# Optimization experiments

Measured on AMD Instinct MI355X. Metric: run time of the kernel, lower is better.

Reference implementation:

```python
import jax, jax.numpy as jnp
import numpy as np

HEAD_SIZE = 128
B, L = 4, 4096

def setup_inputs() -> dict:
    key = jax.random.key(0)
    k1, k2, k3 = jax.random.split(key, 3)
    return {
        "key": jax.random.normal(k1, (B, L, HEAD_SIZE), dtype=jnp.float32),
        "query": jax.random.normal(k2, (B, L, HEAD_SIZE), dtype=jnp.float32),
        "value": jax.random.normal(k3, (B, L, HEAD_SIZE), dtype=jnp.float32),
    }

def reference(key, query, value):
    # attention scores: [B, L, L]
    scale = 1.0 / jnp.sqrt(jnp.asarray(HEAD_SIZE, dtype=query.dtype))
    att = jnp.einsum("bqd,bkd->bqk", query, key) * scale
    # causal mask (tril): positions k > q get -inf
    causal = jnp.tril(jnp.ones((att.shape[1], att.shape[2]), dtype=bool))
    att = jnp.where(causal[None, :, :], att, jnp.array(-jnp.inf, dtype=att.dtype))
    logits = jax.nn.softmax(att, axis=-1)
    # dropout omitted (eval mode / deterministic reference)
    out = jnp.einsum("bqk,bkd->bqd", logits, value)
    return out
```

## Files before the change

kernel.cpp:

```cpp
#include <hip/hip_runtime.h>

#define BB 4
#define LL 4096
#define DD 128

typedef __attribute__((ext_vector_type(8))) short short8;
typedef __attribute__((ext_vector_type(4))) float f32x4;

typedef __attribute__((address_space(1))) const unsigned int gas_u32;
typedef __attribute__((address_space(3))) unsigned int las_u32;

__device__ __forceinline__ void gload_lds16(const void* g, void* l) {
  __builtin_amdgcn_global_load_lds((gas_u32*)g, (las_u32*)l, 16, 0, 0);
}

__device__ __forceinline__ unsigned short f2bf(float x) {
  union { float f; unsigned int u; } c; c.f = x;
  unsigned int r = (c.u + 0x7FFFu + ((c.u >> 16) & 1u)) >> 16;
  return (unsigned short)r;
}
__device__ __forceinline__ float bf2f(unsigned short h) {
  union { unsigned int u; float f; } c; c.u = (unsigned int)h << 16;
  return c.f;
}

__host__ __device__ __forceinline__ int slotBase(int p) {
  int g2 = (p - 4) >> 2, w2 = (p - 4) & 3;
  return 2 * g2 * g2 + 6 * g2 + w2 * (g2 + 2);
}

__global__ __launch_bounds__(256) void prep(const float* __restrict__ K,
                                            const float* __restrict__ V,
                                            unsigned short* __restrict__ Kb,
                                            unsigned short* __restrict__ Vt) {
  __shared__ unsigned short tile[64 * 130];
  int b  = blockIdx.x >> 6;
  int kt = (blockIdx.x & 63) << 6;
  int t = threadIdx.x;
  {
    int key = t >> 2, part = t & 3;
    const float* src = K + ((size_t)b * LL + kt + key) * DD + part * 32;
    unsigned short* dst = Kb + ((size_t)b * LL + kt + key) * DD + part * 32;
#pragma unroll
    for (int j = 0; j < 4; ++j) {
      float4 x = *(const float4*)(src + j * 8);
      float4 y = *(const float4*)(src + j * 8 + 4);
      union { unsigned short h[8]; uint4 v; } o;
      o.h[0] = f2bf(x.x); o.h[1] = f2bf(x.y); o.h[2] = f2bf(x.z); o.h[3] = f2bf(x.w);
      o.h[4] = f2bf(y.x); o.h[5] = f2bf(y.y); o.h[6] = f2bf(y.z); o.h[7] = f2bf(y.w);
      *(uint4*)(dst + j * 8) = o.v;
    }
  }
  int keyi = t >> 5, dim = (t & 31) * 4;
#pragma unroll
  for (int j = 0; j < 8; ++j) {
    int key = keyi + j * 8;
    float4 x = *(const float4*)(V + ((size_t)b * LL + kt + key) * DD + dim);
    uint2 pk;
    pk.x = f2bf(x.x) | ((unsigned int)f2bf(x.y) << 16);
    pk.y = f2bf(x.z) | ((unsigned int)f2bf(x.w) << 16);
    *(uint2*)(tile + key * 130 + dim) = pk;
  }
  __syncthreads();
  int kg = (t & 7) * 8, d0 = t >> 3;
#pragma unroll
  for (int j = 0; j < 4; ++j) {
    int d = d0 + j * 32;
    union { unsigned short h[8]; uint4 v; } o;
#pragma unroll
    for (int i = 0; i < 8; ++i) o.h[i] = tile[(kg + i) * 130 + d];
    *(uint4*)(Vt + ((size_t)b * DD + d) * LL + kt + kg) = o.v;
  }
}

__global__ __launch_bounds__(256, 3) void attn_fwd(const float* __restrict__ Q,
                                                   const unsigned short* __restrict__ Kb,
                                                   const unsigned short* __restrict__ Vt,
                                                   float* __restrict__ Out,
                                                   unsigned short* __restrict__ partO,
                                                   float* __restrict__ stats,
                                                   int split) {
  __shared__ unsigned short Ks[64 * 128];
  __shared__ unsigned short Vs[128 * 64];
  __shared__ unsigned short Ps[4][32 * 72];

  int tid = threadIdx.x;
  int wave = tid >> 6;
  int lane = tid & 63;
  int l = lane & 15, gq = lane >> 4;
  int lx = l & 7;

  int rem = (int)blockIdx.x, p = 31, nch;
  while (true) {
    nch = split ? ((2 * p + 2 + 7) >> 3) : 1;
    int n = 4 * nch;
    if (rem < n) break;
    rem -= n; --p;
  }
  int b = rem / nch, c = rem % nch;
  int T = 2 * p + 2;
  int nIters = split ? min(8, T - c * 8) : T;
  int ktBase = c << 9;
  int q0w = (p << 7) + wave * 32;
  int wkend = q0w + 31;
  int slot = (split && nch > 1) ? (b * 140 + slotBase(p) + c) : 0;

  const float SC = 0.08838834764831845f * 1.4426950408889634f;
  short8 qf[2][4];
#pragma unroll
  for (int mt = 0; mt < 2; ++mt) {
    const float* qp = Q + ((size_t)b * LL + q0w + mt * 16 + l) * DD + gq * 8;
#pragma unroll
    for (int cc = 0; cc < 4; ++cc) {
      float4 x = *(const float4*)(qp + cc * 32);
      float4 y = *(const float4*)(qp + cc * 32 + 4);
      short8 f;
      f[0] = (short)f2bf(x.x * SC); f[1] = (short)f2bf(x.y * SC);
      f[2] = (short)f2bf(x.z * SC); f[3] = (short)f2bf(x.w * SC);
      f[4] = (short)f2bf(y.x * SC); f[5] = (short)f2bf(y.y * SC);
      f[6] = (short)f2bf(y.z * SC); f[7] = (short)f2bf(y.w * SC);
      qf[mt][cc] = f;
    }
  }

  f32x4 acc[2][8];
#pragma unroll
  for (int mt = 0; mt < 2; ++mt)
#pragma unroll
    for (int i = 0; i < 8; ++i) acc[mt][i] = (f32x4){0.f, 0.f, 0.f, 0.f};
  f32x4 den[2];
  den[0] = (f32x4){0.f, 0.f, 0.f, 0.f};
  den[1] = (f32x4){0.f, 0.f, 0.f, 0.f};

  short8 ones;
#pragma unroll
  for (int j = 0; j < 8; ++j) ones[j] = (short)0x3F80;

  unsigned short* Pw = Ps[wave];
  const unsigned short* kgbase = Kb + (size_t)b * LL * DD;
  const unsigned short* vgbase = Vt + (size_t)b * DD * LL;

  for (int it = 0; it < nIters; ++it) {
    int kt = ktBase + it * 64;

    __syncthreads();
#pragma unroll
    for (int j = 0; j < 4; ++j) {
      int pk_ = j * 256 + tid;
      int krow = pk_ >> 4;
      int kcol = (pk_ & 15) ^ (krow & 7);
      gload_lds16(kgbase + (size_t)(kt + krow) * DD + kcol * 8, &Ks[pk_ * 8]);
      int vrow = pk_ >> 3;
      int vcol = (pk_ & 7) ^ (vrow & 7);
      gload_lds16(vgbase + (size_t)vrow * LL + kt + vcol * 8, &Vs[pk_ * 8]);
    }
    __syncthreads();

    if (kt > wkend) continue;

    bool diag = (kt + 63 > q0w);

#pragma unroll
    for (int nt = 0; nt < 4; ++nt) {
      const unsigned short* kp = Ks + (nt * 16 + l) * 128;
      f32x4 a0 = (f32x4){0.f, 0.f, 0.f, 0.f};
      f32x4 a1 = (f32x4){0.f, 0.f, 0.f, 0.f};
#pragma unroll
      for (int cc = 0; cc < 4; ++cc) {
        short8 kf = *(const short8*)(kp + (((gq + 4 * cc) ^ lx) << 3));
        a0 = __builtin_amdgcn_mfma_f32_16x16x32_bf16(qf[0][cc], kf, a0, 0, 0, 0);
        a1 = __builtin_amdgcn_mfma_f32_16x16x32_bf16(qf[1][cc], kf, a1, 0, 0, 0);
      }
      if (diag) {
        int key = kt + nt * 16 + l;
        int qr0 = q0w + gq * 4, qr1 = q0w + 16 + gq * 4;
#pragma unroll
        for (int r = 0; r < 4; ++r) {
          if (key > qr0 + r) a0[r] = -1e30f;
          if (key > qr1 + r) a1[r] = -1e30f;
        }
      }
#pragma unroll
      for (int r = 0; r < 4; ++r) {
        Pw[(gq * 4 + r) * 72 + nt * 16 + l] = f2bf(exp2f(a0[r]));
        Pw[(16 + gq * 4 + r) * 72 + nt * 16 + l] = f2bf(exp2f(a1[r]));
      }
    }

#pragma unroll
    for (int kc = 0; kc < 2; ++kc) {
      short8 pa0 = *(const short8*)(Pw + l * 72 + kc * 32 + gq * 8);
      short8 pa1 = *(const short8*)(Pw + (16 + l) * 72 + kc * 32 + gq * 8);
      den[0] = __builtin_amdgcn_mfma_f32_16x16x32_bf16(pa0, ones, den[0], 0, 0, 0);
      den[1] = __builtin_amdgcn_mfma_f32_16x16x32_bf16(pa1, ones, den[1], 0, 0, 0);
#pragma unroll
      for (int dt = 0; dt < 8; ++dt) {
        short8 vb = *(const short8*)(Vs + (dt * 16 + l) * 64 + (((kc * 4 + gq) ^ lx) << 3));
        acc[0][dt] = __builtin_amdgcn_mfma_f32_16x16x32_bf16(pa0, vb, acc[0][dt], 0, 0, 0);
        acc[1][dt] = __builtin_amdgcn_mfma_f32_16x16x32_bf16(pa1, vb, acc[1][dt], 0, 0, 0);
      }
    }
  }

  if (!split || nch == 1) {
    float* op = Out + ((size_t)b * LL + q0w) * DD;
#pragma unroll
    for (int mt = 0; mt < 2; ++mt) {
      float inv[4];
#pragma unroll
      for (int r = 0; r < 4; ++r) inv[r] = 1.0f / den[mt][r];
#pragma unroll
      for (int dt = 0; dt < 8; ++dt)
#pragma unroll
        for (int r = 0; r < 4; ++r)
          op[(size_t)(mt * 16 + gq * 4 + r) * DD + dt * 16 + l] = acc[mt][dt][r] * inv[r];
    }
  } else {
    unsigned short* pp = partO + (size_t)slot * 16384;
#pragma unroll
    for (int mt = 0; mt < 2; ++mt) {
      int rb = wave * 32 + mt * 16;
#pragma unroll
      for (int dt = 0; dt < 8; ++dt)
#pragma unroll
        for (int r = 0; r < 4; ++r)
          pp[(rb + gq * 4 + r) * 128 + dt * 16 + l] = f2bf(acc[mt][dt][r]);
      if (l == 0) {
#pragma unroll
        for (int r = 0; r < 4; ++r)
          stats[(size_t)slot * 128 + rb + gq * 4 + r] = den[mt][r];
      }
    }
  }
}

__global__ __launch_bounds__(256) void merge(const unsigned short* __restrict__ partO,
                                             const float* __restrict__ stats,
                                             float* __restrict__ Out) {
  int b = blockIdx.x / 112;
  int rest = blockIdx.x % 112;
  int p = 4 + rest / 4;
  int rg = rest % 4;
  int nch = (2 * p + 2 + 7) >> 3;
  int slot0 = b * 140 + slotBase(p);

  int tid = threadIdx.x;
  int row = rg * 32 + (tid >> 3);
  int dcol = (tid & 7) * 16;

  float lsum = 0.f;
  for (int cc = 0; cc < nch; ++cc)
    lsum += stats[(size_t)(slot0 + cc) * 128 + row];
  float inv = 1.0f / lsum;

  float o[16];
#pragma unroll
  for (int j = 0; j < 16; ++j) o[j] = 0.f;
  for (int cc = 0; cc < nch; ++cc) {
    const unsigned short* pp = partO + (size_t)(slot0 + cc) * 16384 + (size_t)row * 128 + dcol;
#pragma unroll
    for (int j = 0; j < 16; ++j) o[j] += bf2f(pp[j]);
  }
  float* op = Out + ((size_t)b * LL + (p << 7) + row) * DD + dcol;
#pragma unroll
  for (int j = 0; j < 4; ++j) {
    float4 v; v.x = o[j*4] * inv; v.y = o[j*4+1] * inv; v.z = o[j*4+2] * inv; v.w = o[j*4+3] * inv;
    *(float4*)(op + j * 4) = v;
  }
}

extern "C" void kernel_launch(void* const* d_in, const int* in_sizes, int n_in,
                              void* d_out, int out_size, void* d_ws, size_t ws_size,
                              hipStream_t stream) {
  const float* K = (const float*)d_in[0];
  const float* Q = (const float*)d_in[1];
  const float* V = (const float*)d_in[2];
  float* Out = (float*)d_out;

  const size_t convBytes = (size_t)2 * BB * LL * DD * 2;
  unsigned short* Kb = (unsigned short*)d_ws;
  unsigned short* Vt = Kb + (size_t)BB * LL * DD;

  size_t slots = (size_t)BB * 140;
  size_t need = convBytes + slots * 16384 * 2 + slots * 128 * 4;
  int split = (ws_size >= need) ? 1 : 0;

  unsigned short* partO = (unsigned short*)((char*)d_ws + convBytes);
  float* stats = (float*)((char*)d_ws + convBytes + slots * 16384 * 2);

  int nBlocks = 0;
  for (int p = 0; p < 32; ++p) nBlocks += 4 * (split ? ((2 * p + 2 + 7) >> 3) : 1);

  prep<<<dim3(BB * (LL / 64)), dim3(256), 0, stream>>>(K, V, Kb, Vt);
  attn_fwd<<<dim3(nBlocks), dim3(256), 0, stream>>>(Q, Kb, Vt, Out, partO, stats, split);
  if (split)
    merge<<<dim3(BB * 112), dim3(256), 0, stream>>>(partO, stats, Out);
}
```

Before: 124.3 us.

## Double-buffer K/V LDS tiles with 32-key steps to overlap loads and compute

Cuts the key tile from 64 to 32 rows and double-buffers the K and V shared-memory tiles. The global-to-LDS load for the next tile is issued before computing on the current one, so each iteration needs one barrier instead of two. The V swizzle and the P buffer stride are changed to fit the 32-wide tile. Total LDS use stays about the same, but there are twice as many iterations and each has a barrier and less MFMA work to hide latency.

```diff
diff --git a/kernel.cpp b/kernel.cpp
--- a/kernel.cpp
+++ b/kernel.cpp
@@ -80,15 +80,16 @@
                                                    unsigned short* __restrict__ partO,
                                                    float* __restrict__ stats,
                                                    int split) {
-  __shared__ unsigned short Ks[64 * 128];
-  __shared__ unsigned short Vs[128 * 64];
-  __shared__ unsigned short Ps[4][32 * 72];
+  __shared__ unsigned short Ks[2][32 * 128];
+  __shared__ unsigned short Vs[2][128 * 32];
+  __shared__ unsigned short Ps[4][32 * 40];
 
   int tid = threadIdx.x;
   int wave = tid >> 6;
   int lane = tid & 63;
   int l = lane & 15, gq = lane >> 4;
   int lx = l & 7;
+  int vsw = (gq ^ ((l >> 1) & 3)) << 3;
 
   int rem = (int)blockIdx.x, p = 31, nch;
   while (true) {
@@ -98,8 +99,8 @@
     rem -= n; --p;
   }
   int b = rem / nch, c = rem % nch;
-  int T = 2 * p + 2;
-  int nIters = split ? min(8, T - c * 8) : T;
+  int T32 = 4 * p + 4;
+  int nIters = split ? min(16, T32 - c * 16) : T32;
   int ktBase = c << 9;
   int q0w = (p << 7) + wave * 32;
   int wkend = q0w + 31;
@@ -140,66 +141,74 @@
   const unsigned short* kgbase = Kb + (size_t)b * LL * DD;
   const unsigned short* vgbase = Vt + (size_t)b * DD * LL;
 
-  for (int it = 0; it < nIters; ++it) {
-    int kt = ktBase + it * 64;
-
-    __syncthreads();
-#pragma unroll
-    for (int j = 0; j < 4; ++j) {
+  auto stage = [&](int kt, int nb) {
+#pragma unroll
+    for (int j = 0; j < 2; ++j) {
       int pk_ = j * 256 + tid;
       int krow = pk_ >> 4;
       int kcol = (pk_ & 15) ^ (krow & 7);
-      gload_lds16(kgbase + (size_t)(kt + krow) * DD + kcol * 8, &Ks[pk_ * 8]);
-      int vrow = pk_ >> 3;
-      int vcol = (pk_ & 7) ^ (vrow & 7);
-      gload_lds16(vgbase + (size_t)vrow * LL + kt + vcol * 8, &Vs[pk_ * 8]);
-    }
-    __syncthreads();
-
-    if (kt > wkend) continue;
-
-    bool diag = (kt + 63 > q0w);
-
-#pragma unroll
-    for (int nt = 0; nt < 4; ++nt) {
-      const unsigned short* kp = Ks + (nt * 16 + l) * 128;
-      f32x4 a0 = (f32x4){0.f, 0.f, 0.f, 0.f};
-      f32x4 a1 = (f32x4){0.f, 0.f, 0.f, 0.f};
-#pragma unroll
-      for (int cc = 0; cc < 4; ++cc) {
-        short8 kf = *(const short8*)(kp + (((gq + 4 * cc) ^ lx) << 3));
-        a0 = __builtin_amdgcn_mfma_f32_16x16x32_bf16(qf[0][cc], kf, a0, 0, 0, 0);
-        a1 = __builtin_amdgcn_mfma_f32_16x16x32_bf16(qf[1][cc], kf, a1, 0, 0, 0);
-      }
-      if (diag) {
-        int key = kt + nt * 16 + l;
-        int qr0 = q0w + gq * 4, qr1 = q0w + 16 + gq * 4;
+      gload_lds16(kgbase + (size_t)(kt + krow) * DD + kcol * 8, &Ks[nb][pk_ * 8]);
+      int vrow = pk_ >> 2;
+      int vcol = (pk_ & 3) ^ ((vrow >> 1) & 3);
+      gload_lds16(vgbase + (size_t)vrow * LL + kt + vcol * 8, &Vs[nb][pk_ * 8]);
+    }
+  };
+
+  stage(ktBase, 0);
+  __syncthreads();
+
+  int cur = 0;
+  for (int it = 0; it < nIters; ++it) {
+    int kt = ktBase + it * 32;
+
+    if (it + 1 < nIters) stage(kt + 32, cur ^ 1);
+
+    if (kt <= wkend) {
+      bool diag = (kt + 31 > q0w);
+      const unsigned short* kbp = Ks[cur];
+      const unsigned short* vbp = Vs[cur];
+
+#pragma unroll
+      for (int nt = 0; nt < 2; ++nt) {
+        const unsigned short* kp = kbp + (nt * 16 + l) * 128;
+        f32x4 a0 = (f32x4){0.f, 0.f, 0.f, 0.f};
+        f32x4 a1 = (f32x4){0.f, 0.f, 0.f, 0.f};
+#pragma unroll
+        for (int cc = 0; cc < 4; ++cc) {
+          short8 kf = *(const short8*)(kp + (((gq + 4 * cc) ^ lx) << 3));
+          a0 = __builtin_amdgcn_mfma_f32_16x16x32_bf16(qf[0][cc], kf, a0, 0, 0, 0);
+          a1 = __builtin_amdgcn_mfma_f32_16x16x32_bf16(qf[1][cc], kf, a1, 0, 0, 0);
+        }
+        if (diag) {
+          int key = kt + nt * 16 + l;
+          int qr0 = q0w + gq * 4, qr1 = q0w + 16 + gq * 4;
+#pragma unroll
+          for (int r = 0; r < 4; ++r) {
+            if (key > qr0 + r) a0[r] = -1e30f;
+            if (key > qr1 + r) a1[r] = -1e30f;
+          }
+        }
 #pragma unroll
         for (int r = 0; r < 4; ++r) {
-          if (key > qr0 + r) a0[r] = -1e30f;
-          if (key > qr1 + r) a1[r] = -1e30f;
+          Pw[(gq * 4 + r) * 40 + nt * 16 + l] = f2bf(exp2f(a0[r]));
+          Pw[(16 + gq * 4 + r) * 40 + nt * 16 + l] = f2bf(exp2f(a1[r]));
         }
       }
-#pragma unroll
-      for (int r = 0; r < 4; ++r) {
-        Pw[(gq * 4 + r) * 72 + nt * 16 + l] = f2bf(exp2f(a0[r]));
-        Pw[(16 + gq * 4 + r) * 72 + nt * 16 + l] = f2bf(exp2f(a1[r]));
-      }
-    }
-
-#pragma unroll
-    for (int kc = 0; kc < 2; ++kc) {
-      short8 pa0 = *(const short8*)(Pw + l * 72 + kc * 32 + gq * 8);
-      short8 pa1 = *(const short8*)(Pw + (16 + l) * 72 + kc * 32 + gq * 8);
+
+      short8 pa0 = *(const short8*)(Pw + l * 40 + gq * 8);
+      short8 pa1 = *(const short8*)(Pw + (16 + l) * 40 + gq * 8);
       den[0] = __builtin_amdgcn_mfma_f32_16x16x32_bf16(pa0, ones, den[0], 0, 0, 0);
       den[1] = __builtin_amdgcn_mfma_f32_16x16x32_bf16(pa1, ones, den[1], 0, 0, 0);
 #pragma unroll
       for (int dt = 0; dt < 8; ++dt) {
-        short8 vb = *(const short8*)(Vs + (dt * 16 + l) * 64 + (((kc * 4 + gq) ^ lx) << 3));
-        acc[0][dt] = __builtin_amdgcn_mfma_f32_16x16x32_bf16(pa0, vb, acc[0][dt], 0, 0, 0);
-        acc[1][dt] = __builtin_amdgcn_mfma_f32_16x16x32_bf16(pa1, vb, acc[1][dt], 0, 0, 0);
+        short8 vv = *(const short8*)(vbp + (dt * 16 + l) * 32 + vsw);
+        acc[0][dt] = __builtin_amdgcn_mfma_f32_16x16x32_bf16(pa0, vv, acc[0][dt], 0, 0, 0);
+        acc[1][dt] = __builtin_amdgcn_mfma_f32_16x16x32_bf16(pa1, vv, acc[1][dt], 0, 0, 0);
       }
     }
+
+    __syncthreads();
+    cur ^= 1;
   }
 
   if (!split || nch == 1) {
```

Result: no change. 122.8 us (-1.2%).
